# Kernel tuning notes

Measured on AMD Instinct MI355X. Metric: run time of the kernel, lower is better.

Reference implementation:

```python
import jax, jax.numpy as jnp
import numpy as np

B, N, C = 8, 2048, 256

def setup_inputs() -> dict:
    key = jax.random.key(0)
    ks = jax.random.split(key, 6)
    corr = jax.random.normal(ks[0], (B, N, N), dtype=jnp.float32)
    feat = jax.random.normal(ks[1], (B, N, C), dtype=jnp.float32)
    histogram = jax.random.uniform(ks[2], (B, N, 1), dtype=jnp.float32)
    mask = jax.random.normal(ks[3], (N, N), dtype=jnp.float32)
    # nn.Linear(C, C) params
    lim = 1.0 / np.sqrt(C)
    v_w = jax.random.uniform(ks[4], (C, C), minval=-lim, maxval=lim, dtype=jnp.float32)
    v_b = jax.random.uniform(ks[5], (C,), minval=-lim, maxval=lim, dtype=jnp.float32)
    return {"corr": corr, "feat": feat, "histogram": histogram, "mask": mask, "v_w": v_w, "v_b": v_b}

def reference(corr, feat, histogram, mask, v_w, v_b):
    # histogram is viewed/expanded in the original but never used downstream.
    # masked softmax over last axis: (b, n, n)
    attn = jax.nn.softmax(corr + mask[None, :, :], axis=-1)
    # v projection: y = feat @ v_w.T + v_b   (b, n, c)
    ref_feat_v = jnp.einsum("bnc,dc->bnd", feat, v_w) + v_b
    # attention output: (b, n, c)
    return jnp.einsum("bnm,bmc->bnc", attn, ref_feat_v)
```

## Files before the change

kernel.cpp:

```cpp
#include <hip/hip_runtime.h>
#include <hip/hip_fp16.h>


#define B_ 8
#define N_ 2048
#define C_ 256

typedef _Float16 half8  __attribute__((ext_vector_type(8)));
typedef _Float16 half4v __attribute__((ext_vector_type(4)));
typedef float    f32x4  __attribute__((ext_vector_type(4)));

__global__ __launch_bounds__(256) void k_convw(const float* __restrict__ w,
                                               _Float16* __restrict__ wh) {
    int i = (blockIdx.x * 256 + threadIdx.x) * 4;
    float4 v = *(const float4*)(w + i);
    half4v h = {(_Float16)v.x, (_Float16)v.y, (_Float16)v.z, (_Float16)v.w};
    *(half4v*)(wh + i) = h;
}

__global__ __launch_bounds__(256) void k_trans(const float* __restrict__ feat,
                                               _Float16* __restrict__ featF) {
    __shared__ _Float16 s[64][68];
    int blk  = blockIdx.x;
    int b    = blk >> 7;
    int tile = blk & 127;
    int n0   = (tile >> 2) << 6;
    int c0   = (tile & 3) << 6;
    int t    = threadIdx.x;

    const float* src = feat + ((size_t)(b * N_ + n0)) * C_ + c0;
#pragma unroll
    for (int i = 0; i < 4; ++i) {
        int idx = i * 256 + t;
        int row = idx >> 4;
        int c4  = (idx & 15) << 2;
        float4 v = *(const float4*)(src + (size_t)row * C_ + c4);
        half4v h = {(_Float16)v.x, (_Float16)v.y, (_Float16)v.z, (_Float16)v.w};
        *(half4v*)&s[row][c4] = h;
    }
    __syncthreads();

    int w = t >> 6, l = t & 63;
    int kk  = w & 1;
    int cb0 = (w >> 1) << 1;
#pragma unroll
    for (int cbi = 0; cbi < 2; ++cbi) {
        int cb = cb0 + cbi;
        half8 v;
#pragma unroll
        for (int j = 0; j < 8; ++j)
            v[j] = s[kk * 32 + ((l >> 4) << 3) + j][(cb << 4) + (l & 15)];
        _Float16* dst = featF +
            (((size_t)((b * 64 + (n0 >> 5) + kk) * 16 + (c0 >> 4) + cb)) * 64 + l) * 8;
        *(half8*)dst = v;
    }
}

__global__ __launch_bounds__(512, 4) void k_attn(const float* __restrict__ corr,
                                                 const float* __restrict__ mask,
                                                 const _Float16* __restrict__ featF,
                                                 _Float16* __restrict__ T) {
    __shared__ _Float16 p_lds[2][32][72];
    __shared__ float rowsum[32];

    const int blk = blockIdx.x;
    const int b   = blk >> 6;
    const int r0  = (blk & 63) * 32;
    const int tg  = threadIdx.x;
    const int w   = tg >> 6, l = tg & 63;
    const int wr  = w >> 2, wc = w & 3;
    const int lrow = l & 15, kch = l >> 4;

    const int srow = tg >> 4;
    const int scol = (tg & 15) << 2;

    const float* pc = corr + ((size_t)(b * N_ + r0 + srow)) * N_ + scol;
    const float* pm = mask + ((size_t)(r0 + srow)) * N_ + scol;
    const _Float16* pfb = featF + (size_t)b * (64 * 16 * 512);

    float rs = 0.0f;
    f32x4 acc[4] = {};

    float4 c0 = *(const float4*)pc;
    float4 m0 = *(const float4*)pm;
    {
        float p0 = __expf(c0.x + m0.x), p1 = __expf(c0.y + m0.y),
              p2 = __expf(c0.z + m0.z), p3 = __expf(c0.w + m0.w);
        rs += (p0 + p1) + (p2 + p3);
        half4v h = {(_Float16)p0, (_Float16)p1, (_Float16)p2, (_Float16)p3};
        *(half4v*)&p_lds[0][srow][scol] = h;
    }
    __syncthreads();

    for (int t = 0; t < 32; ++t) {
        const int cur = t & 1;
        if (t < 31) {
            c0 = *(const float4*)(pc + (t + 1) * 64);
            m0 = *(const float4*)(pm + (t + 1) * 64);
        }
#pragma unroll
        for (int kk = 0; kk < 2; ++kk) {
            half8 pa = *(const half8*)&p_lds[cur][wr * 16 + lrow][kk * 32 + kch * 8];
            const _Float16* pft = pfb + (((size_t)(t * 2 + kk) * 16 + wc * 4) * 64 + l) * 8;
#pragma unroll
            for (int q = 0; q < 4; ++q) {
                half8 bf = *(const half8*)(pft + q * 512);
                acc[q] = __builtin_amdgcn_mfma_f32_16x16x32_f16(pa, bf, acc[q], 0, 0, 0);
            }
        }
        if (t < 31) {
            float p0 = __expf(c0.x + m0.x), p1 = __expf(c0.y + m0.y),
                  p2 = __expf(c0.z + m0.z), p3 = __expf(c0.w + m0.w);
            rs += (p0 + p1) + (p2 + p3);
            half4v h = {(_Float16)p0, (_Float16)p1, (_Float16)p2, (_Float16)p3};
            *(half4v*)&p_lds[cur ^ 1][srow][scol] = h;
        }
        __syncthreads();
    }

    rs += __shfl_xor(rs, 1);
    rs += __shfl_xor(rs, 2);
    rs += __shfl_xor(rs, 4);
    rs += __shfl_xor(rs, 8);
    if ((l & 15) == 0) rowsum[srow] = rs;
    __syncthreads();

    float inv[4];
#pragma unroll
    for (int j = 0; j < 4; ++j) inv[j] = 1.0f / rowsum[wr * 16 + kch * 4 + j];

    _Float16* pT = T + ((size_t)(b * N_ + r0 + wr * 16 + kch * 4)) * C_ + wc * 64 + lrow;
#pragma unroll
    for (int j = 0; j < 4; ++j) {
#pragma unroll
        for (int q = 0; q < 4; ++q) {
            pT[(size_t)j * C_ + q * 16] = (_Float16)(acc[q][j] * inv[j]);
        }
    }
}

__global__ __launch_bounds__(256, 2) void k_out(const _Float16* __restrict__ T,
                                                const _Float16* __restrict__ wh,
                                                const float* __restrict__ v_b,
                                                float* __restrict__ out) {
    const int blk = blockIdx.x;
    const int r0  = blk * 32;
    const int t   = threadIdx.x;
    const int w   = t >> 6, l = t & 63;
    const int wr  = w >> 1, wc = w & 1;
    const int lrow = l & 15, kch = l >> 4;

    const _Float16* pA = T  + ((size_t)(r0 + wr * 16 + lrow)) * C_ + kch * 8;
    const _Float16* pB = wh + ((size_t)(wc * 128 + lrow)) * C_ + kch * 8;

    f32x4 acc[8] = {};
#pragma unroll
    for (int step = 0; step < 8; step++) {
        half8 a = *(const half8*)(pA + step * 32);
#pragma unroll
        for (int q = 0; q < 8; q++) {
            half8 bf = *(const half8*)(pB + step * 32 + (size_t)q * 16 * C_);
            acc[q] = __builtin_amdgcn_mfma_f32_16x16x32_f16(a, bf, acc[q], 0, 0, 0);
        }
    }

    float* pO = out + ((size_t)(r0 + wr * 16 + kch * 4)) * C_ + wc * 128 + lrow;
#pragma unroll
    for (int q = 0; q < 8; q++) {
        float bias = v_b[wc * 128 + q * 16 + lrow];
#pragma unroll
        for (int j = 0; j < 4; j++) {
            pO[(size_t)j * C_ + q * 16] = acc[q][j] + bias;
        }
    }
}

extern "C" void kernel_launch(void* const* d_in, const int* in_sizes, int n_in,
                              void* d_out, int out_size, void* d_ws, size_t ws_size,
                              hipStream_t stream) {
    const float* corr = (const float*)d_in[0];
    const float* feat = (const float*)d_in[1];
    const float* mask = (const float*)d_in[3];
    const float* v_w  = (const float*)d_in[4];
    const float* v_b  = (const float*)d_in[5];
    float* out = (float*)d_out;

    char* ws = (char*)d_ws;
    _Float16* featF = (_Float16*)ws;
    _Float16* T     = (_Float16*)(ws + (size_t)8 * 1024 * 1024);
    _Float16* wh    = (_Float16*)(ws + (size_t)16 * 1024 * 1024);

    hipLaunchKernelGGL(k_trans, dim3(1024), dim3(256), 0, stream, feat, featF);
    hipLaunchKernelGGL(k_convw, dim3(64),   dim3(256), 0, stream, v_w, wh);
    hipLaunchKernelGGL(k_attn,  dim3(512),  dim3(512), 0, stream, corr, mask, featF, T);
    hipLaunchKernelGGL(k_out,   dim3(512),  dim3(256), 0, stream, T, wh, v_b, out);
}
```

Before: 92.38 us.

## Enlarge attention tile to 64 rows and stage feat tiles in LDS via async loads

After: 87.78 us. -5.0%, faster.

```diff
diff --git a/kernel.cpp b/kernel.cpp
--- a/kernel.cpp
+++ b/kernel.cpp
@@ -9,6 +9,13 @@
 typedef _Float16 half8  __attribute__((ext_vector_type(8)));
 typedef _Float16 half4v __attribute__((ext_vector_type(4)));
 typedef float    f32x4  __attribute__((ext_vector_type(4)));
+
+static __device__ __forceinline__ void gload_lds16(const _Float16* g, _Float16* l) {
+    __builtin_amdgcn_global_load_lds(
+        (const __attribute__((address_space(1))) unsigned int*)g,
+        (__attribute__((address_space(3))) unsigned int*)l,
+        16, 0, 0);
+}
 
 __global__ __launch_bounds__(256) void k_convw(const float* __restrict__ w,
                                                _Float16* __restrict__ wh) {
@@ -56,64 +63,78 @@
     }
 }
 
-__global__ __launch_bounds__(512, 4) void k_attn(const float* __restrict__ corr,
-                                                 const float* __restrict__ mask,
-                                                 const _Float16* __restrict__ featF,
-                                                 _Float16* __restrict__ T) {
-    __shared__ _Float16 p_lds[2][32][72];
-    __shared__ float rowsum[32];
-
-    const int blk = blockIdx.x;
-    const int b   = blk >> 6;
-    const int r0  = (blk & 63) * 32;
-    const int tg  = threadIdx.x;
-    const int w   = tg >> 6, l = tg & 63;
-    const int wr  = w >> 2, wc = w & 3;
+__global__ __launch_bounds__(1024, 4) void k_attn(const float* __restrict__ corr,
+                                                  const float* __restrict__ mask,
+                                                  const _Float16* __restrict__ featF,
+                                                  _Float16* __restrict__ T) {
+    __shared__ _Float16 p_lds[2][64][72];
+    __shared__ _Float16 f_lds[2][2][16][64][8];
+    __shared__ float rowsum[64];
+
+    const int rblk = blockIdx.x >> 3;
+    const int b    = blockIdx.x & 7;
+    const int r0   = rblk * 64;
+    const int tg   = threadIdx.x;
+    const int w    = tg >> 6, l = tg & 63;
+    const int wr   = w >> 3, wc = w & 7;
     const int lrow = l & 15, kch = l >> 4;
 
     const int srow = tg >> 4;
     const int scol = (tg & 15) << 2;
 
-    const float* pc = corr + ((size_t)(b * N_ + r0 + srow)) * N_ + scol;
-    const float* pm = mask + ((size_t)(r0 + srow)) * N_ + scol;
+    const float*    pc  = corr + ((size_t)(b * N_ + r0 + srow)) * N_ + scol;
+    const float*    pm  = mask + ((size_t)(r0 + srow)) * N_ + scol;
     const _Float16* pfb = featF + (size_t)b * (64 * 16 * 512);
 
     float rs = 0.0f;
-    f32x4 acc[4] = {};
-
-    float4 c0 = *(const float4*)pc;
-    float4 m0 = *(const float4*)pm;
+    f32x4 acc[2][2] = {};
+
+    float4 cc = *(const float4*)pc;
+    float4 mm = *(const float4*)pm;
     {
-        float p0 = __expf(c0.x + m0.x), p1 = __expf(c0.y + m0.y),
-              p2 = __expf(c0.z + m0.z), p3 = __expf(c0.w + m0.w);
+        float p0 = __expf(cc.x + mm.x), p1 = __expf(cc.y + mm.y),
+              p2 = __expf(cc.z + mm.z), p3 = __expf(cc.w + mm.w);
         rs += (p0 + p1) + (p2 + p3);
         half4v h = {(_Float16)p0, (_Float16)p1, (_Float16)p2, (_Float16)p3};
         *(half4v*)&p_lds[0][srow][scol] = h;
     }
+#pragma unroll
+    for (int i = 0; i < 2; ++i) {
+        int chunk = i * 16 + w;
+        gload_lds16(pfb + chunk * 512 + l * 8, &f_lds[0][0][0][0][0] + chunk * 512);
+    }
     __syncthreads();
 
     for (int t = 0; t < 32; ++t) {
-        const int cur = t & 1;
+        const int cur = t & 1, nxt = cur ^ 1;
         if (t < 31) {
-            c0 = *(const float4*)(pc + (t + 1) * 64);
-            m0 = *(const float4*)(pm + (t + 1) * 64);
+            const _Float16* gsrc = pfb + (size_t)(t + 1) * 16384;
+            _Float16* fdst = &f_lds[nxt][0][0][0][0];
+#pragma unroll
+            for (int i = 0; i < 2; ++i) {
+                int chunk = i * 16 + w;
+                gload_lds16(gsrc + chunk * 512 + l * 8, fdst + chunk * 512);
+            }
+            cc = *(const float4*)(pc + (t + 1) * 64);
+            mm = *(const float4*)(pm + (t + 1) * 64);
         }
 #pragma unroll
         for (int kk = 0; kk < 2; ++kk) {
-            half8 pa = *(const half8*)&p_lds[cur][wr * 16 + lrow][kk * 32 + kch * 8];
-            const _Float16* pft = pfb + (((size_t)(t * 2 + kk) * 16 + wc * 4) * 64 + l) * 8;
-#pragma unroll
-            for (int q = 0; q < 4; ++q) {
-                half8 bf = *(const half8*)(pft + q * 512);
-                acc[q] = __builtin_amdgcn_mfma_f32_16x16x32_f16(pa, bf, acc[q], 0, 0, 0);
-            }
+            half8 a0 = *(const half8*)&p_lds[cur][wr * 32 + lrow][kk * 32 + kch * 8];
+            half8 a1 = *(const half8*)&p_lds[cur][wr * 32 + 16 + lrow][kk * 32 + kch * 8];
+            half8 b0 = *(const half8*)&f_lds[cur][kk][wc * 2][l][0];
+            half8 b1 = *(const half8*)&f_lds[cur][kk][wc * 2 + 1][l][0];
+            acc[0][0] = __builtin_amdgcn_mfma_f32_16x16x32_f16(a0, b0, acc[0][0], 0, 0, 0);
+            acc[0][1] = __builtin_amdgcn_mfma_f32_16x16x32_f16(a0, b1, acc[0][1], 0, 0, 0);
+            acc[1][0] = __builtin_amdgcn_mfma_f32_16x16x32_f16(a1, b0, acc[1][0], 0, 0, 0);
+            acc[1][1] = __builtin_amdgcn_mfma_f32_16x16x32_f16(a1, b1, acc[1][1], 0, 0, 0);
         }
         if (t < 31) {
-            float p0 = __expf(c0.x + m0.x), p1 = __expf(c0.y + m0.y),
-                  p2 = __expf(c0.z + m0.z), p3 = __expf(c0.w + m0.w);
+            float p0 = __expf(cc.x + mm.x), p1 = __expf(cc.y + mm.y),
+                  p2 = __expf(cc.z + mm.z), p3 = __expf(cc.w + mm.w);
             rs += (p0 + p1) + (p2 + p3);
             half4v h = {(_Float16)p0, (_Float16)p1, (_Float16)p2, (_Float16)p3};
-            *(half4v*)&p_lds[cur ^ 1][srow][scol] = h;
+            *(half4v*)&p_lds[nxt][srow][scol] = h;
         }
         __syncthreads();
     }
@@ -125,16 +146,20 @@
     if ((l & 15) == 0) rowsum[srow] = rs;
     __syncthreads();
 
-    float inv[4];
-#pragma unroll
-    for (int j = 0; j < 4; ++j) inv[j] = 1.0f / rowsum[wr * 16 + kch * 4 + j];
-
-    _Float16* pT = T + ((size_t)(b * N_ + r0 + wr * 16 + kch * 4)) * C_ + wc * 64 + lrow;
-#pragma unroll
-    for (int j = 0; j < 4; ++j) {
-#pragma unroll
-        for (int q = 0; q < 4; ++q) {
-            pT[(size_t)j * C_ + q * 16] = (_Float16)(acc[q][j] * inv[j]);
+#pragma unroll
+    for (int m = 0; m < 2; ++m) {
+        float inv[4];
+#pragma unroll
+        for (int j = 0; j < 4; ++j)
+            inv[j] = 1.0f / rowsum[wr * 32 + m * 16 + kch * 4 + j];
+        _Float16* pT = T + ((size_t)(b * N_ + r0 + wr * 32 + m * 16 + kch * 4)) * C_
+                         + wc * 32 + lrow;
+#pragma unroll
+        for (int j = 0; j < 4; ++j) {
+#pragma unroll
+            for (int n = 0; n < 2; ++n) {
+                pT[(size_t)j * C_ + n * 16] = (_Float16)(acc[m][n][j] * inv[j]);
+            }
         }
     }
 }
@@ -192,6 +217,6 @@
 
     hipLaunchKernelGGL(k_trans, dim3(1024), dim3(256), 0, stream, feat, featF);
     hipLaunchKernelGGL(k_convw, dim3(64),   dim3(256), 0, stream, v_w, wh);
-    hipLaunchKernelGGL(k_attn,  dim3(512),  dim3(512), 0, stream, corr, mask, featF, T);
+    hipLaunchKernelGGL(k_attn,  dim3(256),  dim3(1024), 0, stream, corr, mask, featF, T);
     hipLaunchKernelGGL(k_out,   dim3(512),  dim3(256), 0, stream, T, wh, v_b, out);
 }
```

## Restructure attention kernel to per-wave 16-row full-width tiles with split-K

Applied to the files above, without the earlier changes.

New measurement: 96.10 us. +4.0%, slower.

```diff
diff --git a/kernel.cpp b/kernel.cpp
--- a/kernel.cpp
+++ b/kernel.cpp
@@ -56,85 +56,102 @@
     }
 }
 
-__global__ __launch_bounds__(512, 4) void k_attn(const float* __restrict__ corr,
+__global__ __launch_bounds__(128, 2) void k_attn(const float* __restrict__ corr,
                                                  const float* __restrict__ mask,
                                                  const _Float16* __restrict__ featF,
                                                  _Float16* __restrict__ T) {
-    __shared__ _Float16 p_lds[2][32][72];
-    __shared__ float rowsum[32];
+    __shared__ float accL[16 * 260];
+    __shared__ float rsL[16];
 
     const int blk = blockIdx.x;
-    const int b   = blk >> 6;
-    const int r0  = (blk & 63) * 32;
-    const int tg  = threadIdx.x;
-    const int w   = tg >> 6, l = tg & 63;
-    const int wr  = w >> 2, wc = w & 3;
+    const int b   = blk & 7;
+    const int r0  = (blk >> 3) << 4;
+    const int w   = threadIdx.x >> 6;
+    const int l   = threadIdx.x & 63;
     const int lrow = l & 15, kch = l >> 4;
-
-    const int srow = tg >> 4;
-    const int scol = (tg & 15) << 2;
-
-    const float* pc = corr + ((size_t)(b * N_ + r0 + srow)) * N_ + scol;
-    const float* pm = mask + ((size_t)(r0 + srow)) * N_ + scol;
-    const _Float16* pfb = featF + (size_t)b * (64 * 16 * 512);
-
+    const int kb  = w << 10;
+
+    const float* pc = corr + ((size_t)(b * N_ + r0 + lrow)) * N_ + kb + kch * 8;
+    const float* pm = mask + ((size_t)(r0 + lrow)) * N_ + kb + kch * 8;
+    const _Float16* pw = featF + (size_t)b * 524288 + (size_t)(w * 32) * 8192 + l * 8;
+
+    f32x4 acc[16] = {};
     float rs = 0.0f;
-    f32x4 acc[4] = {};
-
-    float4 c0 = *(const float4*)pc;
-    float4 m0 = *(const float4*)pm;
-    {
-        float p0 = __expf(c0.x + m0.x), p1 = __expf(c0.y + m0.y),
-              p2 = __expf(c0.z + m0.z), p3 = __expf(c0.w + m0.w);
-        rs += (p0 + p1) + (p2 + p3);
-        half4v h = {(_Float16)p0, (_Float16)p1, (_Float16)p2, (_Float16)p3};
-        *(half4v*)&p_lds[0][srow][scol] = h;
+
+    half8 bu[16], bv[16];
+#pragma unroll
+    for (int n = 0; n < 16; ++n) bu[n] = *(const half8*)(pw + n * 512);
+
+    float4 cA0 = *(const float4*)pc,        cA1 = *(const float4*)(pc + 4);
+    float4 mA0 = *(const float4*)pm,        mA1 = *(const float4*)(pm + 4);
+    float4 cB0 = *(const float4*)(pc + 32), cB1 = *(const float4*)(pc + 36);
+    float4 mB0 = *(const float4*)(pm + 32), mB1 = *(const float4*)(pm + 36);
+
+#define STEP(T_, CC0, CC1, MM0, MM1, BC, BN)                                  \
+    {                                                                         \
+        const int t_ = (T_);                                                  \
+                             \
+        if (t_ < 31) {                                                        \
+            _Pragma("unroll")                                                 \
+            for (int n = 0; n < 16; ++n)                                      \
+                BN[n] = *(const half8*)(pw + (size_t)(t_ + 1) * 8192 + n * 512); \
+        }                                                                     \
+                              \
+        float e0 = __expf(CC0.x + MM0.x), e1 = __expf(CC0.y + MM0.y);         \
+        float e2 = __expf(CC0.z + MM0.z), e3 = __expf(CC0.w + MM0.w);         \
+        float e4 = __expf(CC1.x + MM1.x), e5 = __expf(CC1.y + MM1.y);         \
+        float e6 = __expf(CC1.z + MM1.z), e7 = __expf(CC1.w + MM1.w);         \
+        rs += ((e0 + e1) + (e2 + e3)) + ((e4 + e5) + (e6 + e7));              \
+        half8 a = {(_Float16)e0, (_Float16)e1, (_Float16)e2, (_Float16)e3,    \
+                   (_Float16)e4, (_Float16)e5, (_Float16)e6, (_Float16)e7};   \
+                        \
+        if (t_ < 30) {                                                        \
+            CC0 = *(const float4*)(pc + (t_ + 2) * 32);                       \
+            CC1 = *(const float4*)(pc + (t_ + 2) * 32 + 4);                   \
+            MM0 = *(const float4*)(pm + (t_ + 2) * 32);                       \
+            MM1 = *(const float4*)(pm + (t_ + 2) * 32 + 4);                   \
+        }                                                                     \
+                                             \
+        _Pragma("unroll")                                                     \
+        for (int n = 0; n < 16; ++n)                                          \
+            acc[n] = __builtin_amdgcn_mfma_f32_16x16x32_f16(a, BC[n], acc[n], 0, 0, 0); \
+    }
+
+    for (int th = 0; th < 16; ++th) {
+        STEP(2 * th,     cA0, cA1, mA0, mA1, bu, bv);
+        STEP(2 * th + 1, cB0, cB1, mB0, mB1, bv, bu);
+    }
+#undef STEP
+
+    rs += __shfl_xor(rs, 16);
+    rs += __shfl_xor(rs, 32);
+
+    if (w == 1) {
+#pragma unroll
+        for (int n = 0; n < 16; ++n) {
+#pragma unroll
+            for (int j = 0; j < 4; ++j)
+                accL[(kch * 4 + j) * 260 + n * 16 + lrow] = acc[n][j];
+        }
+        if (l < 16) rsL[l] = rs;
     }
     __syncthreads();
 
-    for (int t = 0; t < 32; ++t) {
-        const int cur = t & 1;
-        if (t < 31) {
-            c0 = *(const float4*)(pc + (t + 1) * 64);
-            m0 = *(const float4*)(pm + (t + 1) * 64);
-        }
-#pragma unroll
-        for (int kk = 0; kk < 2; ++kk) {
-            half8 pa = *(const half8*)&p_lds[cur][wr * 16 + lrow][kk * 32 + kch * 8];
-            const _Float16* pft = pfb + (((size_t)(t * 2 + kk) * 16 + wc * 4) * 64 + l) * 8;
-#pragma unroll
-            for (int q = 0; q < 4; ++q) {
-                half8 bf = *(const half8*)(pft + q * 512);
-                acc[q] = __builtin_amdgcn_mfma_f32_16x16x32_f16(pa, bf, acc[q], 0, 0, 0);
+    if (w == 0) {
+        float rstot = rs + rsL[lrow];
+        float inv[4];
+#pragma unroll
+        for (int j = 0; j < 4; ++j)
+            inv[j] = 1.0f / __shfl(rstot, kch * 4 + j);
+
+        _Float16* pT = T + ((size_t)(b * N_ + r0 + kch * 4)) * C_ + lrow;
+#pragma unroll
+        for (int n = 0; n < 16; ++n) {
+#pragma unroll
+            for (int j = 0; j < 4; ++j) {
+                float v = acc[n][j] + accL[(kch * 4 + j) * 260 + n * 16 + lrow];
+                pT[(size_t)j * C_ + n * 16] = (_Float16)(v * inv[j]);
             }
-        }
-        if (t < 31) {
-            float p0 = __expf(c0.x + m0.x), p1 = __expf(c0.y + m0.y),
-                  p2 = __expf(c0.z + m0.z), p3 = __expf(c0.w + m0.w);
-            rs += (p0 + p1) + (p2 + p3);
-            half4v h = {(_Float16)p0, (_Float16)p1, (_Float16)p2, (_Float16)p3};
-            *(half4v*)&p_lds[cur ^ 1][srow][scol] = h;
-        }
-        __syncthreads();
-    }
-
-    rs += __shfl_xor(rs, 1);
-    rs += __shfl_xor(rs, 2);
-    rs += __shfl_xor(rs, 4);
-    rs += __shfl_xor(rs, 8);
-    if ((l & 15) == 0) rowsum[srow] = rs;
-    __syncthreads();
-
-    float inv[4];
-#pragma unroll
-    for (int j = 0; j < 4; ++j) inv[j] = 1.0f / rowsum[wr * 16 + kch * 4 + j];
-
-    _Float16* pT = T + ((size_t)(b * N_ + r0 + wr * 16 + kch * 4)) * C_ + wc * 64 + lrow;
-#pragma unroll
-    for (int j = 0; j < 4; ++j) {
-#pragma unroll
-        for (int q = 0; q < 4; ++q) {
-            pT[(size_t)j * C_ + q * 16] = (_Float16)(acc[q][j] * inv[j]);
         }
     }
 }
@@ -192,6 +209,6 @@
 
     hipLaunchKernelGGL(k_trans, dim3(1024), dim3(256), 0, stream, feat, featF);
     hipLaunchKernelGGL(k_convw, dim3(64),   dim3(256), 0, stream, v_w, wh);
-    hipLaunchKernelGGL(k_attn,  dim3(512),  dim3(512), 0, stream, corr, mask, featF, T);
+    hipLaunchKernelGGL(k_attn,  dim3(1024), dim3(128), 0, stream, corr, mask, featF, T);
     hipLaunchKernelGGL(k_out,   dim3(512),  dim3(256), 0, stream, T, wh, v_b, out);
 }
```

## Precompute exp(mask) in fp16 and pipeline attention via direct-to-LDS async loads

Applied to the files above, without the earlier changes.

Result: faster. 87.11 us (-5.7%).

```diff
diff --git a/kernel.cpp b/kernel.cpp
--- a/kernel.cpp
+++ b/kernel.cpp
@@ -9,6 +9,12 @@
 typedef _Float16 half8  __attribute__((ext_vector_type(8)));
 typedef _Float16 half4v __attribute__((ext_vector_type(4)));
 typedef float    f32x4  __attribute__((ext_vector_type(4)));
+
+static __device__ __forceinline__ void gload16(const void* g, void* l) {
+    __builtin_amdgcn_global_load_lds(
+        (const __attribute__((address_space(1))) unsigned int*)g,
+        (__attribute__((address_space(3))) unsigned int*)l, 16, 0, 0);
+}
 
 __global__ __launch_bounds__(256) void k_convw(const float* __restrict__ w,
                                                _Float16* __restrict__ wh) {
@@ -56,85 +62,172 @@
     }
 }
 
-__global__ __launch_bounds__(512, 4) void k_attn(const float* __restrict__ corr,
-                                                 const float* __restrict__ mask,
+__global__ __launch_bounds__(256) void k_expm(const float* __restrict__ mask,
+                                              _Float16* __restrict__ expmF) {
+    __shared__ float s[64][68];
+    int nb4 = blockIdx.x >> 5;
+    int kb2 = blockIdx.x & 31;
+    int t   = threadIdx.x;
+
+    const float* src = mask + ((size_t)(nb4 * 64)) * N_ + kb2 * 64;
+#pragma unroll
+    for (int i = 0; i < 4; ++i) {
+        int idx = i * 256 + t;
+        int row = idx >> 4;
+        int c4  = (idx & 15) << 2;
+        float4 v = *(const float4*)(src + (size_t)row * N_ + c4);
+        s[row][c4 + 0] = __expf(v.x);
+        s[row][c4 + 1] = __expf(v.y);
+        s[row][c4 + 2] = __expf(v.z);
+        s[row][c4 + 3] = __expf(v.w);
+    }
+    __syncthreads();
+
+    int w = t >> 6, l = t & 63;
+#pragma unroll
+    for (int kbl = 0; kbl < 2; ++kbl) {
+        half8 v;
+#pragma unroll
+        for (int j = 0; j < 8; ++j)
+            v[j] = (_Float16)s[w * 16 + (l & 15)][kbl * 32 + ((l >> 4) << 3) + j];
+        _Float16* dst = expmF +
+            (((size_t)(nb4 * 4 + w)) * 64 + kb2 * 2 + kbl) * 512 + l * 8;
+        *(half8*)dst = v;
+    }
+}
+
+__global__ __launch_bounds__(512, 2) void k_attn(const float* __restrict__ corr,
+                                                 const _Float16* __restrict__ expmF,
                                                  const _Float16* __restrict__ featF,
                                                  _Float16* __restrict__ T) {
-    __shared__ _Float16 p_lds[2][32][72];
-    __shared__ float rowsum[32];
+    __shared__ float    c_lds[2][64 * 128];
+    __shared__ _Float16 f_lds[64 * 512];
 
     const int blk = blockIdx.x;
-    const int b   = blk >> 6;
-    const int r0  = (blk & 63) * 32;
+    const int b   = blk & 7;
+    const int sg  = blk >> 3;
+    const int r0  = sg * 64;
     const int tg  = threadIdx.x;
     const int w   = tg >> 6, l = tg & 63;
-    const int wr  = w >> 2, wc = w & 3;
+    const int wr  = w >> 1, wc = w & 1;
     const int lrow = l & 15, kch = l >> 4;
 
-    const int srow = tg >> 4;
-    const int scol = (tg & 15) << 2;
-
-    const float* pc = corr + ((size_t)(b * N_ + r0 + srow)) * N_ + scol;
-    const float* pm = mask + ((size_t)(r0 + srow)) * N_ + scol;
-    const _Float16* pfb = featF + (size_t)b * (64 * 16 * 512);
-
+    const float*    pcorr = corr + ((size_t)(b * N_ + r0)) * N_;
+    const _Float16* pex   = expmF + ((size_t)(sg * 4 + wr)) * 64 * 512 + l * 8;
+    const _Float16* pfb   = featF + (size_t)b * 524288;
+
+    f32x4 acc[8] = {};
     float rs = 0.0f;
-    f32x4 acc[4] = {};
-
-    float4 c0 = *(const float4*)pc;
-    float4 m0 = *(const float4*)pm;
-    {
-        float p0 = __expf(c0.x + m0.x), p1 = __expf(c0.y + m0.y),
-              p2 = __expf(c0.z + m0.z), p3 = __expf(c0.w + m0.w);
-        rs += (p0 + p1) + (p2 + p3);
-        half4v h = {(_Float16)p0, (_Float16)p1, (_Float16)p2, (_Float16)p3};
-        *(half4v*)&p_lds[0][srow][scol] = h;
-    }
-    __syncthreads();
-
-    for (int t = 0; t < 32; ++t) {
-        const int cur = t & 1;
-        if (t < 31) {
-            c0 = *(const float4*)(pc + (t + 1) * 64);
-            m0 = *(const float4*)(pm + (t + 1) * 64);
-        }
-#pragma unroll
-        for (int kk = 0; kk < 2; ++kk) {
-            half8 pa = *(const half8*)&p_lds[cur][wr * 16 + lrow][kk * 32 + kch * 8];
-            const _Float16* pft = pfb + (((size_t)(t * 2 + kk) * 16 + wc * 4) * 64 + l) * 8;
-#pragma unroll
-            for (int q = 0; q < 4; ++q) {
-                half8 bf = *(const half8*)(pft + q * 512);
-                acc[q] = __builtin_amdgcn_mfma_f32_16x16x32_f16(pa, bf, acc[q], 0, 0, 0);
-            }
-        }
-        if (t < 31) {
-            float p0 = __expf(c0.x + m0.x), p1 = __expf(c0.y + m0.y),
-                  p2 = __expf(c0.z + m0.z), p3 = __expf(c0.w + m0.w);
-            rs += (p0 + p1) + (p2 + p3);
-            half4v h = {(_Float16)p0, (_Float16)p1, (_Float16)p2, (_Float16)p3};
-            *(half4v*)&p_lds[cur ^ 1][srow][scol] = h;
-        }
-        __syncthreads();
-    }
-
-    rs += __shfl_xor(rs, 1);
-    rs += __shfl_xor(rs, 2);
-    rs += __shfl_xor(rs, 4);
-    rs += __shfl_xor(rs, 8);
-    if ((l & 15) == 0) rowsum[srow] = rs;
-    __syncthreads();
-
-    float inv[4];
-#pragma unroll
-    for (int j = 0; j < 4; ++j) inv[j] = 1.0f / rowsum[wr * 16 + kch * 4 + j];
-
-    _Float16* pT = T + ((size_t)(b * N_ + r0 + wr * 16 + kch * 4)) * C_ + wc * 64 + lrow;
+
+#define STAGE_CORR(SS)                                                        \
+    { _Pragma("unroll")                                                       \
+      for (int i_ = 0; i_ < 4; ++i_) {                                        \
+        int rpair = w * 8 + i_ * 2;                                           \
+        int row   = rpair + (l >> 5);                                         \
+        int ch    = l & 31;                                                   \
+        int grp   = (ch >> 1) ^ (row & 15);                                   \
+        gload16(pcorr + (size_t)row * N_ + (SS) * 128 + grp * 8 + (ch & 1) * 4, \
+                &c_lds[(SS) & 1][rpair * 128]);                               \
+      } }
+
+#define STAGE_F(SS)                                                           \
+    { _Pragma("unroll")                                                       \
+      for (int i_ = 0; i_ < 8; ++i_) {                                        \
+        int cid = w * 8 + i_;                                                 \
+        gload16(pfb + (((size_t)(SS) * 4 + (cid >> 4)) * 16 + (cid & 15)) * 512 + l * 8, \
+                &f_lds[cid * 512]);                                           \
+      } }
+
+#define SUBSTEP(SSB, SUB, EK0, EK1)                                           \
+    {                                                                         \
+        const float* cl = &c_lds[SSB][(wr * 16 + lrow) * 128];                \
+        int s0 = ((SUB) * 8 + kch) ^ lrow;                                    \
+        int s1 = ((SUB) * 8 + 4 + kch) ^ lrow;                                \
+        f32x4 c00 = *(const f32x4*)(cl + s0 * 8);                             \
+        f32x4 c01 = *(const f32x4*)(cl + s0 * 8 + 4);                         \
+        f32x4 c10 = *(const f32x4*)(cl + s1 * 8);                             \
+        f32x4 c11 = *(const f32x4*)(cl + s1 * 8 + 4);                         \
+        half8 a0, a1;                                                         \
+        _Pragma("unroll")                                                     \
+        for (int j = 0; j < 4; ++j) {                                         \
+            float p0 = __expf(c00[j]) * (float)EK0[j];                        \
+            rs += p0; a0[j] = (_Float16)p0;                                   \
+            float p1 = __expf(c01[j]) * (float)EK0[4 + j];                    \
+            rs += p1; a0[4 + j] = (_Float16)p1;                               \
+            float p2 = __expf(c10[j]) * (float)EK1[j];                        \
+            rs += p2; a1[j] = (_Float16)p2;                                   \
+            float p3 = __expf(c11[j]) * (float)EK1[4 + j];                    \
+            rs += p3; a1[4 + j] = (_Float16)p3;                               \
+        }                                                                     \
+        _Pragma("unroll")                                                     \
+        for (int n = 0; n < 8; ++n) {                                         \
+            half8 b0 = *(const half8*)&f_lds[(((SUB) * 2 + 0) * 16 + wc * 8 + n) * 512 + l * 8]; \
+            half8 b1 = *(const half8*)&f_lds[(((SUB) * 2 + 1) * 16 + wc * 8 + n) * 512 + l * 8]; \
+            acc[n] = __builtin_amdgcn_mfma_f32_16x16x32_f16(a0, b0, acc[n], 0, 0, 0); \
+            acc[n] = __builtin_amdgcn_mfma_f32_16x16x32_f16(a1, b1, acc[n], 0, 0, 0); \
+        }                                                                     \
+    }
+
+#define SSBODY(SS, EC0, EC1, EC2, EC3, EN0, EN1, EN2, EN3)                    \
+    {                                                                         \
+        if ((SS) < 15) { asm volatile("s_waitcnt vmcnt(8)" ::: "memory"); }   \
+        else           { asm volatile("s_waitcnt vmcnt(0)" ::: "memory"); }   \
+        __builtin_amdgcn_sched_barrier(0);                                    \
+        __builtin_amdgcn_s_barrier();                                         \
+        __builtin_amdgcn_sched_barrier(0);                                    \
+        SUBSTEP((SS) & 1, 0, EC0, EC1);                                       \
+        SUBSTEP((SS) & 1, 1, EC2, EC3);                                       \
+        asm volatile("s_waitcnt lgkmcnt(0)" ::: "memory");                    \
+        __builtin_amdgcn_sched_barrier(0);                                    \
+        __builtin_amdgcn_s_barrier();                                         \
+        __builtin_amdgcn_sched_barrier(0);                                    \
+        if ((SS) < 15) {                                                      \
+            STAGE_F((SS) + 1);                                                \
+            __builtin_amdgcn_sched_barrier(0);                                \
+            EN0 = *(const half8*)(pex + (size_t)(4 * (SS) + 4) * 512);        \
+            EN1 = *(const half8*)(pex + (size_t)(4 * (SS) + 5) * 512);        \
+            EN2 = *(const half8*)(pex + (size_t)(4 * (SS) + 6) * 512);        \
+            EN3 = *(const half8*)(pex + (size_t)(4 * (SS) + 7) * 512);        \
+            __builtin_amdgcn_sched_barrier(0);                                \
+            if ((SS) < 14) STAGE_CORR((SS) + 2);                              \
+            __builtin_amdgcn_sched_barrier(0);                                \
+        }                                                                     \
+    }
+
+    half8 eA0, eA1, eA2, eA3, eB0, eB1, eB2, eB3;
+    STAGE_CORR(0);
+    __builtin_amdgcn_sched_barrier(0);
+    STAGE_F(0);
+    __builtin_amdgcn_sched_barrier(0);
+    eA0 = *(const half8*)(pex + (size_t)0 * 512);
+    eA1 = *(const half8*)(pex + (size_t)1 * 512);
+    eA2 = *(const half8*)(pex + (size_t)2 * 512);
+    eA3 = *(const half8*)(pex + (size_t)3 * 512);
+    __builtin_amdgcn_sched_barrier(0);
+    STAGE_CORR(1);
+    __builtin_amdgcn_sched_barrier(0);
+
+    for (int sh = 0; sh < 8; ++sh) {
+        SSBODY(2 * sh,     eA0, eA1, eA2, eA3, eB0, eB1, eB2, eB3);
+        SSBODY(2 * sh + 1, eB0, eB1, eB2, eB3, eA0, eA1, eA2, eA3);
+    }
+#undef SSBODY
+#undef SUBSTEP
+#undef STAGE_F
+#undef STAGE_CORR
+
+    rs += __shfl_xor(rs, 16);
+    rs += __shfl_xor(rs, 32);
+    float inv = 1.0f / rs;
+
+    _Float16* pT = T + ((size_t)(b * N_ + r0 + wr * 16 + kch * 4)) * C_
+                     + wc * 128 + lrow;
 #pragma unroll
     for (int j = 0; j < 4; ++j) {
-#pragma unroll
-        for (int q = 0; q < 4; ++q) {
-            pT[(size_t)j * C_ + q * 16] = (_Float16)(acc[q][j] * inv[j]);
+        float invj = __shfl(inv, kch * 4 + j);
+#pragma unroll
+        for (int n = 0; n < 8; ++n) {
+            pT[(size_t)j * C_ + n * 16] = (_Float16)(acc[n][j] * invj);
         }
     }
 }
@@ -189,9 +282,11 @@
     _Float16* featF = (_Float16*)ws;
     _Float16* T     = (_Float16*)(ws + (size_t)8 * 1024 * 1024);
     _Float16* wh    = (_Float16*)(ws + (size_t)16 * 1024 * 1024);
+    _Float16* expmF = (_Float16*)(ws + (size_t)17 * 1024 * 1024);
 
     hipLaunchKernelGGL(k_trans, dim3(1024), dim3(256), 0, stream, feat, featF);
+    hipLaunchKernelGGL(k_expm,  dim3(1024), dim3(256), 0, stream, mask, expmF);
     hipLaunchKernelGGL(k_convw, dim3(64),   dim3(256), 0, stream, v_w, wh);
-    hipLaunchKernelGGL(k_attn,  dim3(512),  dim3(512), 0, stream, corr, mask, featF, T);
+    hipLaunchKernelGGL(k_attn,  dim3(256),  dim3(512), 0, stream, corr, expmF, featF, T);
     hipLaunchKernelGGL(k_out,   dim3(512),  dim3(256), 0, stream, T, wh, v_b, out);
 }
```
